# Performance work log

Measured on AMD Instinct MI355X. Metric: run time of the kernel, lower is better.

Reference implementation:

```python
import jax, jax.numpy as jnp
import numpy as np

B, T, D, H = 2, 2048, 1024, 16
DK = D // H  # 64

def setup_inputs() -> dict:
    key = jax.random.key(0)
    ks = jax.random.split(key, 8)
    s = 1.0 / np.sqrt(D)
    return {
        'q': jax.random.normal(ks[0], (B, T, D), jnp.float32),
        'k': jax.random.normal(ks[1], (B, T, D), jnp.float32),
        'v': jax.random.normal(ks[2], (B, T, D), jnp.float32),
        'Wq': jax.random.normal(ks[3], (D, D), jnp.float32) * s,
        'bq': jnp.zeros((D,), jnp.float32),
        'Wk': jax.random.normal(ks[4], (D, D), jnp.float32) * s,
        'bk': jnp.zeros((D,), jnp.float32),
        'Wv': jax.random.normal(ks[5], (D, DK), jnp.float32) * s,
        'bv': jnp.zeros((DK,), jnp.float32),
        'Wo': jax.random.normal(ks[6], (DK, D), jnp.float32) * (1.0 / np.sqrt(DK)),
        'bo': jnp.zeros((D,), jnp.float32),
    }

def reference(q, k, v, Wq, bq, Wk, bk, Wv, bv, Wo, bo):
    Bq, Tq, _ = q.shape
    # projections; split heads: [B,T,H,dk]
    Q = (q @ Wq + bq).reshape(Bq, Tq, H, DK)
    K = (k @ Wk + bk).reshape(Bq, Tq, H, DK)
    V = v @ Wv + bv  # [B,T,dk] shared across heads
    scores = jnp.einsum('bthd,bshd->bhts', Q, K) / np.sqrt(DK)
    attn = jax.nn.softmax(scores, axis=-1)          # [B,H,T,T] (dropout=0 in eval)
    attn_mean = attn.mean(axis=1)                   # [B,T,T]
    # V shared across heads => mean_h(attn_h @ V) == attn_mean @ V
    context = jnp.einsum('bts,bsd->btd', attn_mean, V)  # [B,T,dk]
    out = context @ Wo + bo                         # [B,T,D]
    return out, attn_mean
```

## Files before the change

kernel.cpp:

```cpp
#include <hip/hip_runtime.h>
#include <hip/hip_bf16.h>

constexpr int B_  = 2;
constexpr int T_  = 2048;
constexpr int D_  = 1024;
constexpr int H_  = 16;
constexpr int DK_ = 64;
#define SC_EXP 0.18033688011112042591f

typedef __attribute__((ext_vector_type(8))) short bhalf8;
typedef __attribute__((ext_vector_type(4))) float f32x4;

__device__ __forceinline__ f32x4 mfma16(bhalf8 a, bhalf8 b, f32x4 c) {
  return __builtin_amdgcn_mfma_f32_16x16x32_bf16(a, b, c, 0, 0, 0);
}

__device__ __forceinline__ void g2l16(const void* g, void* l) {
  __builtin_amdgcn_global_load_lds((const __attribute__((address_space(1))) void*)g,
                                   (__attribute__((address_space(3))) void*)l, 16, 0, 0);
}

template<int NWG>
__device__ __forceinline__ int xcd_swz(int bid) {
  return (bid & 7) * (NWG / 8) + (bid >> 3);
}

template<int ROWS, int NT>
__device__ __forceinline__ void stage_swz(const char* gbase, int gstride,
                                          char* lds, int tid) {
  const int wave = tid >> 6;
  constexpr int CHUNKS = ROWS * 8;
  #pragma unroll
  for (int j = 0; j < CHUNKS / NT; ++j) {
    int c = j * NT + tid;
    int row = c >> 3, slot = c & 7;
    g2l16(gbase + (size_t)row * gstride + ((slot ^ (row & 7)) << 4),
          lds + (j * NT + wave * 64) * 16);
  }
}

__device__ __forceinline__ bhalf8 frag_ld(const char* tile, int row, int kbyte, int lane) {
  int r = row + (lane & 15);
  int off = kbyte + ((lane >> 4) << 4);
  off ^= (r & 7) << 4;
  return *(const bhalf8*)(tile + r * 128 + off);
}

__device__ __forceinline__ void cvt8_store(char* lds, int row, int slot, const float* f) {
  union { bhalf8 v; __hip_bfloat16 h[8]; } u;
  #pragma unroll
  for (int i = 0; i < 8; ++i) u.h[i] = __float2bfloat16(f[i]);
  *(bhalf8*)(lds + row * 128 + ((slot ^ (row & 7)) << 4)) = u.v;
}

__global__ __launch_bounds__(256) void cast3_bf16(const float* __restrict__ s0,
    const float* __restrict__ s1, const float* __restrict__ s2,
    __hip_bfloat16* __restrict__ d0, __hip_bfloat16* __restrict__ d1,
    __hip_bfloat16* __restrict__ d2, int n8) {
  const float* s = blockIdx.y == 0 ? s0 : blockIdx.y == 1 ? s1 : s2;
  __hip_bfloat16* d = blockIdx.y == 0 ? d0 : blockIdx.y == 1 ? d1 : d2;
  int i = blockIdx.x * 256 + threadIdx.x;
  if (i >= n8) return;
  const float4* sp = (const float4*)(s + (size_t)i * 8);
  float4 f0 = sp[0], f1 = sp[1];
  union { bhalf8 v; __hip_bfloat16 h[8]; } u;
  u.h[0] = __float2bfloat16(f0.x); u.h[1] = __float2bfloat16(f0.y);
  u.h[2] = __float2bfloat16(f0.z); u.h[3] = __float2bfloat16(f0.w);
  u.h[4] = __float2bfloat16(f1.x); u.h[5] = __float2bfloat16(f1.y);
  u.h[6] = __float2bfloat16(f1.z); u.h[7] = __float2bfloat16(f1.w);
  *(bhalf8*)(d + (size_t)i * 8) = u.v;
}

__global__ __launch_bounds__(256) void transpose4_bf16(
    const float* __restrict__ Wq, const float* __restrict__ Wk,
    const float* __restrict__ Wo, const float* __restrict__ Wv,
    __hip_bfloat16* __restrict__ Wqt, __hip_bfloat16* __restrict__ Wkt,
    __hip_bfloat16* __restrict__ Wot, __hip_bfloat16* __restrict__ Wvt) {
  __shared__ float t[32][33];
  const int z = blockIdx.z;
  const float* src = z == 0 ? Wq : z == 1 ? Wk : z == 2 ? Wo : Wv;
  __hip_bfloat16* dst = z == 0 ? Wqt : z == 1 ? Wkt : z == 2 ? Wot : Wvt;
  const int R = (z == 2) ? 64 : 1024;
  const int C = (z == 3) ? 64 : 1024;
  const int tx = threadIdx.x & 31, ty = threadIdx.x >> 5;
  const int c0 = blockIdx.x * 32, r0 = blockIdx.y * 32;
  if (c0 >= C || r0 >= R) return;
  #pragma unroll
  for (int i = 0; i < 32; i += 8)
    t[ty + i][tx] = src[(size_t)(r0 + ty + i) * C + c0 + tx];
  __syncthreads();
  #pragma unroll
  for (int i = 0; i < 32; i += 8)
    dst[(size_t)(c0 + ty + i) * R + r0 + tx] = __float2bfloat16(t[tx][ty + i]);
}

__global__ __launch_bounds__(256) void proj_qk(const __hip_bfloat16* __restrict__ qb,
    const __hip_bfloat16* __restrict__ kb, const __hip_bfloat16* __restrict__ Wqt,
    const __hip_bfloat16* __restrict__ Wkt, const float* __restrict__ bq,
    const float* __restrict__ bk, __hip_bfloat16* __restrict__ Qb,
    __hip_bfloat16* __restrict__ Kb) {
  __shared__ char At[2][128 * 128];
  __shared__ char Bt[2][128 * 128];
  const bool isk = blockIdx.z != 0;
  const __hip_bfloat16* A  = isk ? kb : qb;
  const __hip_bfloat16* Wt = isk ? Wkt : Wqt;
  const float* bias        = isk ? bk : bq;
  __hip_bfloat16* C        = isk ? Kb : Qb;
  const float scale        = isk ? 1.0f : SC_EXP;
  const int tid = threadIdx.x, lane = tid & 63, wave = tid >> 6;
  const int id = xcd_swz<256>(blockIdx.x);
  const int m0 = (id & 31) * 128, n0 = (id >> 5) * 128;
  const int wr = (wave >> 1) * 64, wc = (wave & 1) * 64;
  f32x4 acc[4][4] = {};
  stage_swz<128, 256>((const char*)(A + (size_t)m0 * D_), D_ * 2, At[0], tid);
  stage_swz<128, 256>((const char*)(Wt + (size_t)n0 * D_), D_ * 2, Bt[0], tid);
  __syncthreads();
  int cur = 0;
  for (int k0 = 0; k0 < 16; ++k0) {
    if (k0 + 1 < 16) {
      stage_swz<128, 256>((const char*)(A + (size_t)m0 * D_ + (k0 + 1) * 64), D_ * 2, At[cur ^ 1], tid);
      stage_swz<128, 256>((const char*)(Wt + (size_t)n0 * D_ + (k0 + 1) * 64), D_ * 2, Bt[cur ^ 1], tid);
    }
    bhalf8 a[4], b[4];
    #pragma unroll
    for (int mi = 0; mi < 4; ++mi) {
      a[mi] = frag_ld(At[cur], wr + mi * 16, 0, lane);
      b[mi] = frag_ld(Bt[cur], wc + mi * 16, 0, lane);
    }
    #pragma unroll
    for (int mi = 0; mi < 4; ++mi)
      #pragma unroll
      for (int ni = 0; ni < 4; ++ni)
        acc[mi][ni] = mfma16(a[mi], b[ni], acc[mi][ni]);
    #pragma unroll
    for (int mi = 0; mi < 4; ++mi) {
      a[mi] = frag_ld(At[cur], wr + mi * 16, 64, lane);
      b[mi] = frag_ld(Bt[cur], wc + mi * 16, 64, lane);
    }
    #pragma unroll
    for (int mi = 0; mi < 4; ++mi)
      #pragma unroll
      for (int ni = 0; ni < 4; ++ni)
        acc[mi][ni] = mfma16(a[mi], b[ni], acc[mi][ni]);
    __syncthreads();
    cur ^= 1;
  }
  const int g = lane >> 4, cl = lane & 15;
  #pragma unroll
  for (int ni = 0; ni < 4; ++ni) {
    float bv = bias[n0 + wc + ni * 16 + cl];
    #pragma unroll
    for (int mi = 0; mi < 4; ++mi)
      #pragma unroll
      for (int r = 0; r < 4; ++r) {
        int m = m0 + wr + mi * 16 + g * 4 + r;
        int n = n0 + wc + ni * 16 + cl;
        C[(size_t)m * D_ + n] = __float2bfloat16((acc[mi][ni][r] + bv) * scale);
      }
  }
}

__global__ __launch_bounds__(256) void proj_v_mfma(const __hip_bfloat16* __restrict__ vb,
    const __hip_bfloat16* __restrict__ Wvt, float* __restrict__ Vf_part) {
  __shared__ char At[2][128 * 128];
  __shared__ char Bt[2][64 * 128];
  const int tid = threadIdx.x, lane = tid & 63, wave = tid >> 6;
  const int m0 = blockIdx.x * 128;
  const int k0base = blockIdx.y * 128;
  const int wr = (wave >> 1) * 64, wc = (wave & 1) * 32;
  stage_swz<128, 256>((const char*)(vb + (size_t)m0 * D_ + k0base), D_ * 2, At[0], tid);
  stage_swz<128, 256>((const char*)(vb + (size_t)m0 * D_ + k0base + 64), D_ * 2, At[1], tid);
  stage_swz<64, 256>((const char*)(Wvt + k0base), D_ * 2, Bt[0], tid);
  stage_swz<64, 256>((const char*)(Wvt + k0base + 64), D_ * 2, Bt[1], tid);
  __syncthreads();
  f32x4 acc[4][2] = {};
  #pragma unroll
  for (int kk = 0; kk < 2; ++kk) {
    bhalf8 a[4][2], bb[2][2];
    #pragma unroll
    for (int mi = 0; mi < 4; ++mi)
      #pragma unroll
      for (int ks = 0; ks < 2; ++ks)
        a[mi][ks] = frag_ld(At[kk], wr + mi * 16, ks * 64, lane);
    #pragma unroll
    for (int ni = 0; ni < 2; ++ni)
      #pragma unroll
      for (int ks = 0; ks < 2; ++ks)
        bb[ni][ks] = frag_ld(Bt[kk], wc + ni * 16, ks * 64, lane);
    #pragma unroll
    for (int mi = 0; mi < 4; ++mi)
      #pragma unroll
      for (int ni = 0; ni < 2; ++ni) {
        acc[mi][ni] = mfma16(a[mi][0], bb[ni][0], acc[mi][ni]);
        acc[mi][ni] = mfma16(a[mi][1], bb[ni][1], acc[mi][ni]);
      }
  }
  float* dst = Vf_part + (size_t)blockIdx.y * (B_ * T_ * DK_);
  const int g = lane >> 4, cl = lane & 15;
  #pragma unroll
  for (int mi = 0; mi < 4; ++mi)
    #pragma unroll
    for (int ni = 0; ni < 2; ++ni)
      #pragma unroll
      for (int r = 0; r < 4; ++r) {
        int m = m0 + wr + mi * 16 + g * 4 + r;
        int n = wc + ni * 16 + cl;
        dst[(size_t)m * DK_ + n] = acc[mi][ni][r];
      }
}

__global__ __launch_bounds__(256) void vt_finalize(const float* __restrict__ Vf_part,
    const float* __restrict__ bv, __hip_bfloat16* __restrict__ Vt) {
  __shared__ float t[32][33];
  const int tx = threadIdx.x & 31, ty = threadIdx.x >> 5;
  const int c0 = blockIdx.x * 32, r0 = blockIdx.y * 32;
  #pragma unroll
  for (int i = 0; i < 32; i += 8) {
    size_t idx = (size_t)(r0 + ty + i) * DK_ + c0 + tx;
    float s = bv[c0 + tx];
    #pragma unroll
    for (int p = 0; p < 8; ++p)
      s += Vf_part[idx + (size_t)p * (B_ * T_ * DK_)];
    t[ty + i][tx] = s;
  }
  __syncthreads();
  #pragma unroll
  for (int i = 0; i < 32; i += 8)
    Vt[(size_t)(c0 + ty + i) * (B_ * T_) + r0 + tx] = __float2bfloat16(t[tx][ty + i]);
}

__global__ __launch_bounds__(256) void attn_pass1(const __hip_bfloat16* __restrict__ Qb,
    const __hip_bfloat16* __restrict__ Kb, float* __restrict__ Linv) {
  __shared__ char Qt[128 * 128];
  __shared__ char Kt[2][64 * 128];
  __shared__ float partial[2][128];
  const int tid = threadIdx.x, lane = tid & 63, wave = tid >> 6;
  const int id = xcd_swz<512>(blockIdx.x);
  const int rt = id & 15, h = (id >> 4) & 15, b = id >> 8;
  const int row0 = rt * 128;
  const int wr = (wave >> 1) * 64;
  const int wcid = wave & 1, wc = wcid * 32;
  stage_swz<128, 256>((const char*)(Qb + ((size_t)(b * T_ + row0) * D_ + h * DK_)), D_ * 2, Qt, tid);
  stage_swz<64, 256>((const char*)(Kb + ((size_t)(b * T_) * D_ + h * DK_)), D_ * 2, Kt[0], tid);
  __syncthreads();
  float rs[16] = {};
  int cur = 0;
  for (int ci = 0; ci < 32; ++ci) {
    if (ci + 1 < 32)
      stage_swz<64, 256>((const char*)(Kb + ((size_t)(b * T_ + (ci + 1) * 64) * D_ + h * DK_)),
                         D_ * 2, Kt[cur ^ 1], tid);
    bhalf8 a[4][2], bb[2][2];
    #pragma unroll
    for (int mi = 0; mi < 4; ++mi)
      #pragma unroll
      for (int ks = 0; ks < 2; ++ks)
        a[mi][ks] = frag_ld(Qt, wr + mi * 16, ks * 64, lane);
    #pragma unroll
    for (int ni = 0; ni < 2; ++ni)
      #pragma unroll
      for (int ks = 0; ks < 2; ++ks)
        bb[ni][ks] = frag_ld(Kt[cur], wc + ni * 16, ks * 64, lane);
    #pragma unroll
    for (int mi = 0; mi < 4; ++mi)
      #pragma unroll
      for (int ni = 0; ni < 2; ++ni) {
        f32x4 s = {0.f, 0.f, 0.f, 0.f};
        s = mfma16(a[mi][0], bb[ni][0], s);
        s = mfma16(a[mi][1], bb[ni][1], s);
        #pragma unroll
        for (int r = 0; r < 4; ++r)
          rs[mi * 4 + r] += __builtin_amdgcn_exp2f(s[r]);
      }
    __syncthreads();
    cur ^= 1;
  }
  #pragma unroll
  for (int off = 1; off < 16; off <<= 1)
    #pragma unroll
    for (int i = 0; i < 16; ++i)
      rs[i] += __shfl_xor(rs[i], off, 64);
  if ((lane & 15) == 0) {
    int g = lane >> 4;
    #pragma unroll
    for (int mi = 0; mi < 4; ++mi)
      #pragma unroll
      for (int r = 0; r < 4; ++r)
        partial[wcid][wr + mi * 16 + g * 4 + r] = rs[mi * 4 + r];
  }
  __syncthreads();
  if (tid < 128) {
    float s = partial[0][tid] + partial[1][tid];
    Linv[(size_t)(b * H_ + h) * T_ + row0 + tid] = 1.0f / (16.0f * s);
  }
}

__global__ __launch_bounds__(512) void attn_pass2(const __hip_bfloat16* __restrict__ Qb,
    const __hip_bfloat16* __restrict__ Kb, const float* __restrict__ Linv,
    float* __restrict__ am, __hip_bfloat16* __restrict__ amb) {
  __shared__ char Qt[2][128 * 128];
  __shared__ char Kt[2][128 * 128];
  __shared__ float linv[H_][128];
  const int tid = threadIdx.x, lane = tid & 63, wave = tid >> 6;
  const int id = xcd_swz<512>(blockIdx.x);
  const int col0 = (id & 15) * 128, row0 = ((id >> 4) & 15) * 128, b = id >> 8;
  const int wr = (wave >> 1) * 32, wc = (wave & 1) * 64;
  const int g = lane >> 4, cl = lane & 15;
  for (int i = tid; i < H_ * 128; i += 512) {
    int hh = i >> 7, r = i & 127;
    linv[hh][r] = Linv[(size_t)(b * H_ + hh) * T_ + row0 + r];
  }
  stage_swz<128, 512>((const char*)(Qb + ((size_t)(b * T_ + row0) * D_)), D_ * 2, Qt[0], tid);
  stage_swz<128, 512>((const char*)(Kb + ((size_t)(b * T_ + col0) * D_)), D_ * 2, Kt[0], tid);
  __syncthreads();
  f32x4 acc[2][4] = {};
  int cur = 0;
  for (int h = 0; h < H_; ++h) {
    if (h + 1 < H_) {
      stage_swz<128, 512>((const char*)(Qb + ((size_t)(b * T_ + row0) * D_ + (h + 1) * DK_)),
                          D_ * 2, Qt[cur ^ 1], tid);
      stage_swz<128, 512>((const char*)(Kb + ((size_t)(b * T_ + col0) * D_ + (h + 1) * DK_)),
                          D_ * 2, Kt[cur ^ 1], tid);
    }
    bhalf8 a[2][2], bb[4][2];
    #pragma unroll
    for (int mi = 0; mi < 2; ++mi)
      #pragma unroll
      for (int ks = 0; ks < 2; ++ks)
        a[mi][ks] = frag_ld(Qt[cur], wr + mi * 16, ks * 64, lane);
    #pragma unroll
    for (int ni = 0; ni < 4; ++ni)
      #pragma unroll
      for (int ks = 0; ks < 2; ++ks)
        bb[ni][ks] = frag_ld(Kt[cur], wc + ni * 16, ks * 64, lane);
    #pragma unroll
    for (int mi = 0; mi < 2; ++mi) {
      f32x4 lv = *(const f32x4*)&linv[h][wr + mi * 16 + g * 4];
      #pragma unroll
      for (int ni = 0; ni < 4; ++ni) {
        f32x4 s = {0.f, 0.f, 0.f, 0.f};
        s = mfma16(a[mi][0], bb[ni][0], s);
        s = mfma16(a[mi][1], bb[ni][1], s);
        #pragma unroll
        for (int r = 0; r < 4; ++r)
          acc[mi][ni][r] += __builtin_amdgcn_exp2f(s[r]) * lv[r];
      }
    }
    __syncthreads();
    cur ^= 1;
  }
  #pragma unroll
  for (int mi = 0; mi < 2; ++mi)
    #pragma unroll
    for (int ni = 0; ni < 4; ++ni)
      #pragma unroll
      for (int r = 0; r < 4; ++r) {
        int m = row0 + wr + mi * 16 + g * 4 + r;
        int n = col0 + wc + ni * 16 + cl;
        size_t idx = ((size_t)(b * T_ + m)) * T_ + n;
        am[idx]  = acc[mi][ni][r];
        amb[idx] = __float2bfloat16(acc[mi][ni][r]);
      }
}

__global__ __launch_bounds__(256) void context_gemm(const __hip_bfloat16* __restrict__ amb,
    const __hip_bfloat16* __restrict__ Vt, float* __restrict__ ctx_part) {
  __shared__ char At[2][128 * 128];
  __shared__ char Bt[2][64 * 128];
  const int tid = threadIdx.x, lane = tid & 63, wave = tid >> 6;
  const int m0 = blockIdx.x * 128;
  const int b = m0 >> 11;
  const int k0base = blockIdx.y * 256;
  const int wr = (wave >> 1) * 64, wc = (wave & 1) * 32;
  f32x4 acc[4][2] = {};
  stage_swz<128, 256>((const char*)(amb + (size_t)m0 * T_ + k0base), T_ * 2, At[0], tid);
  stage_swz<64, 256>((const char*)(Vt + (size_t)b * T_ + k0base), B_ * T_ * 2, Bt[0], tid);
  __syncthreads();
  int cur = 0;
  for (int i = 0; i < 4; ++i) {
    if (i + 1 < 4) {
      int kcol = k0base + (i + 1) * 64;
      stage_swz<128, 256>((const char*)(amb + (size_t)m0 * T_ + kcol), T_ * 2, At[cur ^ 1], tid);
      stage_swz<64, 256>((const char*)(Vt + (size_t)b * T_ + kcol), B_ * T_ * 2, Bt[cur ^ 1], tid);
    }
    bhalf8 a[4][2], bb[2][2];
    #pragma unroll
    for (int mi = 0; mi < 4; ++mi)
      #pragma unroll
      for (int ks = 0; ks < 2; ++ks)
        a[mi][ks] = frag_ld(At[cur], wr + mi * 16, ks * 64, lane);
    #pragma unroll
    for (int ni = 0; ni < 2; ++ni)
      #pragma unroll
      for (int ks = 0; ks < 2; ++ks)
        bb[ni][ks] = frag_ld(Bt[cur], wc + ni * 16, ks * 64, lane);
    #pragma unroll
    for (int mi = 0; mi < 4; ++mi)
      #pragma unroll
      for (int ni = 0; ni < 2; ++ni) {
        acc[mi][ni] = mfma16(a[mi][0], bb[ni][0], acc[mi][ni]);
        acc[mi][ni] = mfma16(a[mi][1], bb[ni][1], acc[mi][ni]);
      }
    __syncthreads();
    cur ^= 1;
  }
  float* dst = ctx_part + (size_t)blockIdx.y * (B_ * T_ * DK_);
  const int g = lane >> 4, cl = lane & 15;
  #pragma unroll
  for (int mi = 0; mi < 4; ++mi)
    #pragma unroll
    for (int ni = 0; ni < 2; ++ni)
      #pragma unroll
      for (int r = 0; r < 4; ++r) {
        int m = m0 + wr + mi * 16 + g * 4 + r;
        int n = wc + ni * 16 + cl;
        dst[(size_t)m * DK_ + n] = acc[mi][ni][r];
      }
}

__global__ __launch_bounds__(256) void out_gemm(const float* __restrict__ ctx_part,
    const __hip_bfloat16* __restrict__ Wot, const float* __restrict__ bo,
    float* __restrict__ out) {
  __shared__ char At[128 * 128];
  __shared__ char Bt[128 * 128];
  const int tid = threadIdx.x, lane = tid & 63, wave = tid >> 6;
  const int m0 = blockIdx.x * 128, n0 = blockIdx.y * 128;
  const int wr = (wave >> 1) * 64, wc = (wave & 1) * 64;
  #pragma unroll
  for (int j = 0; j < 4; ++j) {
    int c = tid + j * 256;
    int row = c >> 3, slot = c & 7;
    size_t base = (size_t)(m0 + row) * DK_ + slot * 8;
    float f[8] = {};
    #pragma unroll
    for (int p = 0; p < 8; ++p) {
      const float* src = ctx_part + base + (size_t)p * (B_ * T_ * DK_);
      float4 s0 = *(const float4*)src;
      float4 s1 = *(const float4*)(src + 4);
      f[0] += s0.x; f[1] += s0.y; f[2] += s0.z; f[3] += s0.w;
      f[4] += s1.x; f[5] += s1.y; f[6] += s1.z; f[7] += s1.w;
    }
    cvt8_store(At, row, slot, f);
  }
  stage_swz<128, 256>((const char*)(Wot + (size_t)n0 * DK_), DK_ * 2, Bt, tid);
  __syncthreads();
  bhalf8 a[4][2], bb[4][2];
  #pragma unroll
  for (int mi = 0; mi < 4; ++mi)
    #pragma unroll
    for (int ks = 0; ks < 2; ++ks) {
      a[mi][ks]  = frag_ld(At, wr + mi * 16, ks * 64, lane);
      bb[mi][ks] = frag_ld(Bt, wc + mi * 16, ks * 64, lane);
    }
  f32x4 acc[4][4] = {};
  #pragma unroll
  for (int mi = 0; mi < 4; ++mi)
    #pragma unroll
    for (int ni = 0; ni < 4; ++ni) {
      acc[mi][ni] = mfma16(a[mi][0], bb[ni][0], acc[mi][ni]);
      acc[mi][ni] = mfma16(a[mi][1], bb[ni][1], acc[mi][ni]);
    }
  const int g = lane >> 4, cl = lane & 15;
  #pragma unroll
  for (int ni = 0; ni < 4; ++ni) {
    float bias = bo[n0 + wc + ni * 16 + cl];
    #pragma unroll
    for (int mi = 0; mi < 4; ++mi)
      #pragma unroll
      for (int r = 0; r < 4; ++r) {
        int m = m0 + wr + mi * 16 + g * 4 + r;
        int n = n0 + wc + ni * 16 + cl;
        out[(size_t)m * D_ + n] = acc[mi][ni][r] + bias;
      }
  }
}

extern "C" void kernel_launch(void* const* d_in, const int* in_sizes, int n_in,
                              void* d_out, int out_size, void* d_ws, size_t ws_size,
                              hipStream_t stream) {
  (void)in_sizes; (void)n_in; (void)out_size; (void)ws_size;
  const float* q  = (const float*)d_in[0];
  const float* k  = (const float*)d_in[1];
  const float* v  = (const float*)d_in[2];
  const float* Wq = (const float*)d_in[3];
  const float* bq = (const float*)d_in[4];
  const float* Wk = (const float*)d_in[5];
  const float* bk = (const float*)d_in[6];
  const float* Wv = (const float*)d_in[7];
  const float* bv = (const float*)d_in[8];
  const float* Wo = (const float*)d_in[9];
  const float* bo = (const float*)d_in[10];
  float* out = (float*)d_out;
  float* am  = out + (size_t)B_ * T_ * D_;

  char* p = (char*)d_ws;
  __hip_bfloat16* qb  = (__hip_bfloat16*)p; p += (size_t)B_ * T_ * D_ * 2;
  __hip_bfloat16* kb  = (__hip_bfloat16*)p; p += (size_t)B_ * T_ * D_ * 2;
  __hip_bfloat16* vb  = (__hip_bfloat16*)p; p += (size_t)B_ * T_ * D_ * 2;
  __hip_bfloat16* Qb  = (__hip_bfloat16*)p; p += (size_t)B_ * T_ * D_ * 2;
  __hip_bfloat16* Kb  = (__hip_bfloat16*)p; p += (size_t)B_ * T_ * D_ * 2;
  __hip_bfloat16* Wqt = (__hip_bfloat16*)p; p += (size_t)D_ * D_ * 2;
  __hip_bfloat16* Wkt = (__hip_bfloat16*)p; p += (size_t)D_ * D_ * 2;
  __hip_bfloat16* Wot = (__hip_bfloat16*)p; p += (size_t)D_ * DK_ * 2;
  __hip_bfloat16* Wvt = (__hip_bfloat16*)p; p += (size_t)D_ * DK_ * 2;
  __hip_bfloat16* Vt  = (__hip_bfloat16*)p; p += (size_t)DK_ * B_ * T_ * 2;
  __hip_bfloat16* amb = (__hip_bfloat16*)p; p += (size_t)B_ * T_ * T_ * 2;
  float* Linv     = (float*)p; p += (size_t)B_ * H_ * T_ * 4;
  float* ctx_part = (float*)p; p += (size_t)8 * B_ * T_ * DK_ * 4;
  float* Vf_part  = (float*)p; p += (size_t)8 * B_ * T_ * DK_ * 4;

  const int n8 = B_ * T_ * D_ / 8;
  cast3_bf16<<<dim3(n8 / 256, 3), 256, 0, stream>>>(q, k, v, qb, kb, vb, n8);
  transpose4_bf16<<<dim3(32, 32, 4), 256, 0, stream>>>(Wq, Wk, Wo, Wv, Wqt, Wkt, Wot, Wvt);

  proj_qk<<<dim3(256, 1, 2), 256, 0, stream>>>(qb, kb, Wqt, Wkt, bq, bk, Qb, Kb);
  proj_v_mfma<<<dim3(32, 8), 256, 0, stream>>>(vb, Wvt, Vf_part);
  vt_finalize<<<dim3(2, 128), 256, 0, stream>>>(Vf_part, bv, Vt);

  attn_pass1<<<dim3(512), 256, 0, stream>>>(Qb, Kb, Linv);
  attn_pass2<<<dim3(512), 512, 0, stream>>>(Qb, Kb, Linv, am, amb);

  context_gemm<<<dim3(32, 8), 256, 0, stream>>>(amb, Vt, ctx_part);
  out_gemm<<<dim3(32, 8), 256, 0, stream>>>(ctx_part, Wot, bo, out);
}
```

Baseline: 143.0 us.

## Fuse attn_mean @ V context GEMM into attention pass2 epilogue

The attn_pass2 kernel now stores its averaged attention tile as bf16 into shared memory (reusing the Q buffers) and multiplies it by a staged V tile (reusing the K buffers). It writes per-column-block partial context sums, so the separate context_gemm launch and the bf16 attn_mean round trip to global memory go away. The cost is that partials grow from 8 to 16 slices, which out_gemm must now reduce, and pass2 gains an extra epilogue, shared-memory traffic and register pressure. A launch-bounds occupancy hint is also added.

```diff
diff --git a/kernel.cpp b/kernel.cpp
--- a/kernel.cpp
+++ b/kernel.cpp
@@ -294,9 +294,10 @@
   }
 }
 
-__global__ __launch_bounds__(512) void attn_pass2(const __hip_bfloat16* __restrict__ Qb,
+__global__ __launch_bounds__(512, 4) void attn_pass2(const __hip_bfloat16* __restrict__ Qb,
     const __hip_bfloat16* __restrict__ Kb, const float* __restrict__ Linv,
-    float* __restrict__ am, __hip_bfloat16* __restrict__ amb) {
+    const __hip_bfloat16* __restrict__ Vt, float* __restrict__ am,
+    float* __restrict__ ctx_part) {
   __shared__ char Qt[2][128 * 128];
   __shared__ char Kt[2][128 * 128];
   __shared__ float linv[H_][128];
@@ -348,72 +349,52 @@
     __syncthreads();
     cur ^= 1;
   }
+  stage_swz<64, 512>((const char*)Vt + (size_t)(b * T_ + col0) * 2, B_ * T_ * 2, Kt[0], tid);
+  stage_swz<64, 512>((const char*)Vt + (size_t)(b * T_ + col0 + 64) * 2, B_ * T_ * 2, Kt[1], tid);
   #pragma unroll
   for (int mi = 0; mi < 2; ++mi)
     #pragma unroll
     for (int ni = 0; ni < 4; ++ni)
       #pragma unroll
       for (int r = 0; r < 4; ++r) {
-        int m = row0 + wr + mi * 16 + g * 4 + r;
-        int n = col0 + wc + ni * 16 + cl;
-        size_t idx = ((size_t)(b * T_ + m)) * T_ + n;
-        am[idx]  = acc[mi][ni][r];
-        amb[idx] = __float2bfloat16(acc[mi][ni][r]);
-      }
-}
-
-__global__ __launch_bounds__(256) void context_gemm(const __hip_bfloat16* __restrict__ amb,
-    const __hip_bfloat16* __restrict__ Vt, float* __restrict__ ctx_part) {
-  __shared__ char At[2][128 * 128];
-  __shared__ char Bt[2][64 * 128];
-  const int tid = threadIdx.x, lane = tid & 63, wave = tid >> 6;
-  const int m0 = blockIdx.x * 128;
-  const int b = m0 >> 11;
-  const int k0base = blockIdx.y * 256;
-  const int wr = (wave >> 1) * 64, wc = (wave & 1) * 32;
-  f32x4 acc[4][2] = {};
-  stage_swz<128, 256>((const char*)(amb + (size_t)m0 * T_ + k0base), T_ * 2, At[0], tid);
-  stage_swz<64, 256>((const char*)(Vt + (size_t)b * T_ + k0base), B_ * T_ * 2, Bt[0], tid);
-  __syncthreads();
-  int cur = 0;
-  for (int i = 0; i < 4; ++i) {
-    if (i + 1 < 4) {
-      int kcol = k0base + (i + 1) * 64;
-      stage_swz<128, 256>((const char*)(amb + (size_t)m0 * T_ + kcol), T_ * 2, At[cur ^ 1], tid);
-      stage_swz<64, 256>((const char*)(Vt + (size_t)b * T_ + kcol), B_ * T_ * 2, Bt[cur ^ 1], tid);
-    }
-    bhalf8 a[4][2], bb[2][2];
-    #pragma unroll
-    for (int mi = 0; mi < 4; ++mi)
-      #pragma unroll
-      for (int ks = 0; ks < 2; ++ks)
-        a[mi][ks] = frag_ld(At[cur], wr + mi * 16, ks * 64, lane);
+        int row = wr + mi * 16 + g * 4 + r;
+        int colL = wc + ni * 16 + cl;
+        float v = acc[mi][ni][r];
+        am[((size_t)(b * T_ + row0 + row)) * T_ + col0 + colL] = v;
+        char* base = (colL & 64) ? Qt[1] : Qt[0];
+        int within = colL & 63;
+        int slot = within >> 3;
+        *(__hip_bfloat16*)(base + row * 128 + (((slot ^ (row & 7)) << 4) | ((within & 7) * 2)))
+            = __float2bfloat16(v);
+      }
+  __syncthreads();
+  const int wr2 = (wave >> 1) * 32, wc2 = (wave & 1) * 32;
+  f32x4 acc2[2][2] = {};
+  #pragma unroll
+  for (int mi = 0; mi < 2; ++mi) {
+    bhalf8 pa[4];
+    #pragma unroll
+    for (int kk = 0; kk < 4; ++kk)
+      pa[kk] = frag_ld(Qt[kk >> 1], wr2 + mi * 16, (kk & 1) * 64, lane);
+    #pragma unroll
+    for (int ni = 0; ni < 2; ++ni) {
+      #pragma unroll
+      for (int kk = 0; kk < 4; ++kk) {
+        bhalf8 pv = frag_ld(Kt[kk >> 1], wc2 + ni * 16, (kk & 1) * 64, lane);
+        acc2[mi][ni] = mfma16(pa[kk], pv, acc2[mi][ni]);
+      }
+    }
+  }
+  float* dst = ctx_part + (size_t)(id & 15) * (B_ * T_ * DK_);
+  #pragma unroll
+  for (int mi = 0; mi < 2; ++mi)
     #pragma unroll
     for (int ni = 0; ni < 2; ++ni)
       #pragma unroll
-      for (int ks = 0; ks < 2; ++ks)
-        bb[ni][ks] = frag_ld(Bt[cur], wc + ni * 16, ks * 64, lane);
-    #pragma unroll
-    for (int mi = 0; mi < 4; ++mi)
-      #pragma unroll
-      for (int ni = 0; ni < 2; ++ni) {
-        acc[mi][ni] = mfma16(a[mi][0], bb[ni][0], acc[mi][ni]);
-        acc[mi][ni] = mfma16(a[mi][1], bb[ni][1], acc[mi][ni]);
-      }
-    __syncthreads();
-    cur ^= 1;
-  }
-  float* dst = ctx_part + (size_t)blockIdx.y * (B_ * T_ * DK_);
-  const int g = lane >> 4, cl = lane & 15;
-  #pragma unroll
-  for (int mi = 0; mi < 4; ++mi)
-    #pragma unroll
-    for (int ni = 0; ni < 2; ++ni)
-      #pragma unroll
       for (int r = 0; r < 4; ++r) {
-        int m = m0 + wr + mi * 16 + g * 4 + r;
-        int n = wc + ni * 16 + cl;
-        dst[(size_t)m * DK_ + n] = acc[mi][ni][r];
+        int m = row0 + wr2 + mi * 16 + g * 4 + r;
+        int n = wc2 + ni * 16 + cl;
+        dst[(size_t)(b * T_ + m) * DK_ + n] = acc2[mi][ni][r];
       }
 }
 
@@ -432,7 +413,7 @@
     size_t base = (size_t)(m0 + row) * DK_ + slot * 8;
     float f[8] = {};
     #pragma unroll
-    for (int p = 0; p < 8; ++p) {
+    for (int p = 0; p < 16; ++p) {
       const float* src = ctx_part + base + (size_t)p * (B_ * T_ * DK_);
       float4 s0 = *(const float4*)src;
       float4 s1 = *(const float4*)(src + 4);
@@ -503,9 +484,8 @@
   __hip_bfloat16* Wot = (__hip_bfloat16*)p; p += (size_t)D_ * DK_ * 2;
   __hip_bfloat16* Wvt = (__hip_bfloat16*)p; p += (size_t)D_ * DK_ * 2;
   __hip_bfloat16* Vt  = (__hip_bfloat16*)p; p += (size_t)DK_ * B_ * T_ * 2;
-  __hip_bfloat16* amb = (__hip_bfloat16*)p; p += (size_t)B_ * T_ * T_ * 2;
   float* Linv     = (float*)p; p += (size_t)B_ * H_ * T_ * 4;
-  float* ctx_part = (float*)p; p += (size_t)8 * B_ * T_ * DK_ * 4;
+  float* ctx_part = (float*)p; p += (size_t)16 * B_ * T_ * DK_ * 4;
   float* Vf_part  = (float*)p; p += (size_t)8 * B_ * T_ * DK_ * 4;
 
   const int n8 = B_ * T_ * D_ / 8;
@@ -517,8 +497,7 @@
   vt_finalize<<<dim3(2, 128), 256, 0, stream>>>(Vf_part, bv, Vt);
 
   attn_pass1<<<dim3(512), 256, 0, stream>>>(Qb, Kb, Linv);
-  attn_pass2<<<dim3(512), 512, 0, stream>>>(Qb, Kb, Linv, am, amb);
-
-  context_gemm<<<dim3(32, 8), 256, 0, stream>>>(amb, Vt, ctx_part);
+  attn_pass2<<<dim3(512), 512, 0, stream>>>(Qb, Kb, Linv, Vt, am, ctx_part);
+
   out_gemm<<<dim3(32, 8), 256, 0, stream>>>(ctx_part, Wot, bo, out);
 }
```

Result: faster. 139.3 us (-2.6%).
